# Performance work log

Hardware: AMD Instinct MI355X
Metric: run time of the kernel (lower is better)

## Reference

```python
import jax, jax.numpy as jnp
import numpy as np

EPS = 1e-8  # torch F.cosine_similarity eps


def _gather(features, idx):
    # batched_index_select_tensor: per-batch gather along seq dim
    return jnp.take_along_axis(features, idx[:, :, None], axis=1)


def setup_inputs() -> dict:
    key = jax.random.key(0)
    ks = jax.random.split(key, 7)
    B, S, H, Q, D, C = 8, 512, 768, 64, 256, 2
    return {
        "features": jax.random.normal(ks[0], (B, S, H), dtype=jnp.float32),
        "text_a_indices": jax.random.randint(ks[1], (B, Q), 0, S),
        "text_b_indices": jax.random.randint(ks[2], (B, D), 0, S),
        "W1": jax.random.normal(ks[3], (2 * H, H), dtype=jnp.float32) * 0.02,
        "b1": jax.random.normal(ks[4], (H,), dtype=jnp.float32) * 0.02,
        "W2": jax.random.normal(ks[5], (H, C), dtype=jnp.float32) * 0.02,
        "b2": jax.random.normal(ks[6], (C,), dtype=jnp.float32) * 0.02,
    }


def reference(features, text_a_indices, text_b_indices, W1, b1, W2, b2):
    dt = features.dtype
    a_mask = (text_a_indices > 0).astype(dt)          # [B,Q]
    b_mask = (text_b_indices > 0).astype(dt)          # [B,D]
    a_len = jnp.sum(a_mask, axis=-1)                  # [B]
    b_len = jnp.sum(b_mask, axis=-1)                  # [B]

    q_vec = _gather(features, text_a_indices)         # [B,Q,H]
    d_vec = _gather(features, text_b_indices)         # [B,D,H]

    # cosine similarity with torch eps semantics: x.y / (max(|x|,eps)*max(|y|,eps))
    qn = q_vec / jnp.maximum(jnp.linalg.norm(q_vec, axis=-1, keepdims=True), EPS)
    dn = d_vec / jnp.maximum(jnp.linalg.norm(d_vec, axis=-1, keepdims=True), EPS)
    sim = jnp.einsum("bqh,bdh->bqd", qn, dn)          # [B,Q,D]

    # masked weighted average over doc tokens, per query token (fused; no 4D repeat)
    sim_m = sim * b_mask[:, None, :]
    per_q_doc = jnp.einsum("bqd,bdh->bqh", sim_m, d_vec) / b_len[:, None, None]

    # masked average over query tokens
    am = a_mask[:, :, None]
    query_based_doc = jnp.sum(per_q_doc * am, axis=1) / a_len[:, None]   # [B,H]
    query_avg = jnp.sum(q_vec * am, axis=1) / a_len[:, None]             # [B,H]

    feat = jnp.concatenate([query_avg, query_based_doc], axis=-1)        # [B,2H]
    hidden = jax.nn.relu(feat @ W1 + b1)
    logits = hidden @ W2 + b2
    return logits
```

## Files before the change

### kernel.cpp

```cpp
#include <hip/hip_runtime.h>
#include <hip/hip_bf16.h>

#define B_ 8
#define S_ 512
#define H_ 768
#define Q_ 64
#define D_ 256

__global__ __launch_bounds__(256) void k_norms_lens(
        const float* __restrict__ feats,
        const int* __restrict__ aidx,
        const int* __restrict__ bidx,
        float* __restrict__ invn ,
        float* __restrict__ lens ) {
    int t = threadIdx.x;
    int wave = t >> 6, lane = t & 63;
    if (blockIdx.x < 640) {
        int r = blockIdx.x * 4 + wave;
        int b = r / (Q_ + D_);
        int i = r % (Q_ + D_);
        int idx; float* outp;
        if (i < Q_) {
            idx = aidx[b * Q_ + i];
            outp = invn + b * Q_ + i;
        } else {
            int j = i - Q_;
            idx = bidx[b * D_ + j];
            outp = invn + B_ * Q_ + b * D_ + j;
        }
        const float4* row4 = (const float4*)(feats + ((size_t)b * S_ + idx) * H_);
        float ss = 0.f;
#pragma unroll
        for (int k = 0; k < 3; ++k) {
            float4 v = row4[lane + k * 64];
            ss += v.x * v.x + v.y * v.y + v.z * v.z + v.w * v.w;
        }
        for (int off = 32; off; off >>= 1) ss += __shfl_xor(ss, off, 64);
        if (lane == 0) *outp = 1.f / fmaxf(sqrtf(ss), 1e-8f);
    } else {
        int b = blockIdx.x - 640;
        __shared__ int cnt[4];
        unsigned long long mb = __ballot(bidx[b * D_ + wave * 64 + lane] > 0);
        if (lane == 0) cnt[wave] = __popcll(mb);
        if (wave == 0) {
            unsigned long long ma = __ballot(aidx[b * Q_ + lane] > 0);
            if (lane == 0) lens[b] = (float)__popcll(ma);
        }
        __syncthreads();
        if (t == 0) lens[B_ + b] = (float)(cnt[0] + cnt[1] + cnt[2] + cnt[3]);
    }
}

__global__ __launch_bounds__(256) void k_qbar(
        const float* __restrict__ feats,
        const int* __restrict__ aidx,
        const float* __restrict__ invn,
        const float* __restrict__ lens,
        float* __restrict__ qbar ,
        float* __restrict__ feat ) {
    int b = blockIdx.x / 12;
    int hc = blockIdx.x % 12;
    int t = threadIdx.x;
    int lane = t & 63, qg = t >> 6;
    __shared__ int   s_idx[Q_];
    __shared__ float s_inv[Q_];
    __shared__ float red0[4][64];
    __shared__ float red1[4][64];
    if (t < Q_) {
        s_idx[t] = aidx[b * Q_ + t];
        s_inv[t] = invn[b * Q_ + t];
    }
    __syncthreads();
    int h = hc * 64 + lane;
    float pb = 0.f, pa = 0.f;
#pragma unroll
    for (int q = qg * 16; q < qg * 16 + 16; ++q) {
        int idx = s_idx[q];
        if (idx > 0) {
            float f = feats[((size_t)b * S_ + idx) * H_ + h];
            pb += f * s_inv[q];
            pa += f;
        }
    }
    red0[qg][lane] = pb;
    red1[qg][lane] = pa;
    __syncthreads();
    if (t < 64) {
        int h2 = hc * 64 + t;
        float qb = red0[0][t] + red0[1][t] + red0[2][t] + red0[3][t];
        float qa = red1[0][t] + red1[1][t] + red1[2][t] + red1[3][t];
        qbar[b * H_ + h2] = qb;
        feat[b * 2 * H_ + h2] = qa / lens[b];
    }
}

__global__ __launch_bounds__(256) void k_docw(
        const float* __restrict__ feats,
        const int* __restrict__ bidx,
        const float* __restrict__ invn,
        const float* __restrict__ lens,
        const float* __restrict__ qbar,
        float* __restrict__ w ) {
    int t = threadIdx.x;
    int lane = t & 63;
    int gw = blockIdx.x * 4 + (t >> 6);
    int b = gw >> 8;
    int d = gw & 255;
    int idx = bidx[b * D_ + d];
    const float4* row4 = (const float4*)(feats + ((size_t)b * S_ + idx) * H_);
    const float4* q4 = (const float4*)(qbar + b * H_);
    float dot = 0.f;
#pragma unroll
    for (int k = 0; k < 3; ++k) {
        float4 v = row4[lane + k * 64];
        float4 qv = q4[lane + k * 64];
        dot += v.x * qv.x + v.y * qv.y + v.z * qv.z + v.w * qv.w;
    }
    for (int off = 32; off; off >>= 1) dot += __shfl_xor(dot, off, 64);
    if (lane == 0) {
        float scale = 1.f / (lens[b] * lens[B_ + b]);
        w[b * D_ + d] = (idx > 0) ? dot * invn[B_ * Q_ + b * D_ + d] * scale : 0.f;
    }
}

__global__ __launch_bounds__(256) void k_docsum(
        const float* __restrict__ feats,
        const int* __restrict__ bidx,
        const float* __restrict__ w,
        float* __restrict__ feat) {
    int b = blockIdx.x / 12;
    int hc = blockIdx.x % 12;
    int t = threadIdx.x;
    int lane = t & 63, dg = t >> 6;
    __shared__ float s_w[D_];
    __shared__ int   s_i[D_];
    __shared__ float red[4][64];
    s_w[t] = w[b * D_ + t];
    s_i[t] = bidx[b * D_ + t];
    __syncthreads();
    int h = hc * 64 + lane;
    float acc = 0.f;
#pragma unroll 8
    for (int d = dg * 64; d < dg * 64 + 64; ++d) {
        acc += s_w[d] * feats[((size_t)b * S_ + s_i[d]) * H_ + h];
    }
    red[dg][lane] = acc;
    __syncthreads();
    if (t < 64) {
        feat[b * 2 * H_ + H_ + hc * 64 + t] =
            red[0][t] + red[1][t] + red[2][t] + red[3][t];
    }
}

__global__ __launch_bounds__(256) void k_mlp1(
        const float* __restrict__ feat,
        const float* __restrict__ W1,
        const float* __restrict__ b1,
        float* __restrict__ hidden) {
    int b = blockIdx.x / 12;
    int hc = blockIdx.x % 12;
    int t = threadIdx.x;
    int lane = t & 63, kg = t >> 6;
    __shared__ float s_f[2 * H_];
    __shared__ float red[4][64];
    for (int i = t; i < 2 * H_; i += 256) s_f[i] = feat[b * 2 * H_ + i];
    __syncthreads();
    int h = hc * 64 + lane;
    const float* wp = W1 + (size_t)(kg * 384) * H_ + h;
    const float* fp = s_f + kg * 384;
    float acc = 0.f;
#pragma unroll 8
    for (int k = 0; k < 384; ++k) acc += fp[k] * wp[(size_t)k * H_];
    red[kg][lane] = acc;
    __syncthreads();
    if (t < 64) {
        int h2 = hc * 64 + t;
        float v = red[0][t] + red[1][t] + red[2][t] + red[3][t] + b1[h2];
        hidden[b * H_ + h2] = fmaxf(v, 0.f);
    }
}

__global__ __launch_bounds__(256) void k_mlp2(
        const float* __restrict__ hidden,
        const float* __restrict__ W2,
        const float* __restrict__ b2,
        float* __restrict__ out) {
    int b = blockIdx.x;
    int t = threadIdx.x;
    int lane = t & 63, wave = t >> 6;
    float a0 = 0.f, a1 = 0.f;
#pragma unroll
    for (int k = 0; k < 3; ++k) {
        int h = t + k * 256;
        float v = hidden[b * H_ + h];
        a0 += v * W2[h * 2 + 0];
        a1 += v * W2[h * 2 + 1];
    }
    for (int off = 32; off; off >>= 1) {
        a0 += __shfl_xor(a0, off, 64);
        a1 += __shfl_xor(a1, off, 64);
    }
    __shared__ float r0[4], r1[4];
    if (lane == 0) { r0[wave] = a0; r1[wave] = a1; }
    __syncthreads();
    if (t == 0) {
        out[b * 2 + 0] = r0[0] + r0[1] + r0[2] + r0[3] + b2[0];
        out[b * 2 + 1] = r1[0] + r1[1] + r1[2] + r1[3] + b2[1];
    }
}

extern "C" void kernel_launch(void* const* d_in, const int* in_sizes, int n_in,
                              void* d_out, int out_size, void* d_ws, size_t ws_size,
                              hipStream_t stream) {
    const float* feats = (const float*)d_in[0];
    const int*   aidx  = (const int*)d_in[1];
    const int*   bidx  = (const int*)d_in[2];
    const float* W1    = (const float*)d_in[3];
    const float* b1    = (const float*)d_in[4];
    const float* W2    = (const float*)d_in[5];
    const float* b2    = (const float*)d_in[6];
    float* out = (float*)d_out;

    float* ws = (float*)d_ws;
    float* invn   = ws;
    float* lens   = invn + B_ * (Q_ + D_);
    float* qbar   = lens + 2 * B_;
    float* feat   = qbar + B_ * H_;
    float* w      = feat + B_ * 2 * H_;
    float* hidden = w + B_ * D_;

    k_norms_lens<<<648, 256, 0, stream>>>(feats, aidx, bidx, invn, lens);
    k_qbar<<<96, 256, 0, stream>>>(feats, aidx, invn, lens, qbar, feat);
    k_docw<<<512, 256, 0, stream>>>(feats, bidx, invn, lens, qbar, w);
    k_docsum<<<96, 256, 0, stream>>>(feats, bidx, w, feat);
    k_mlp1<<<96, 256, 0, stream>>>(feat, W1, b1, hidden);
    k_mlp2<<<B_, 256, 0, stream>>>(hidden, W2, b2, out);
}
```

Measured before the change: 114.1 us.

## Fuse six-kernel pipeline into one cooperative kernel with grid-wide syncs

Replaces the chain of six small kernel launches with a single cooperative kernel of 640 blocks that runs each stage in turn, separated by grid.sync(), with shared memory reused through a union. The second MLP layer is folded into the first by reducing within a wavefront and adding atomically into a zeroed output. This targets per-launch overhead and inter-kernel gaps in a tiny, latency-bound workload. In exchange it adds grid barrier cost, atomics that make the summation order nondeterministic, and relies on 640 co-resident blocks, falling back to the old launches if the cooperative launch fails.

New measurement: 396.1 us. 3.47x slower.

```diff
diff --git a/kernel.cpp b/kernel.cpp
--- a/kernel.cpp
+++ b/kernel.cpp
@@ -1,5 +1,8 @@
 #include <hip/hip_runtime.h>
+#include <hip/hip_cooperative_groups.h>
 #include <hip/hip_bf16.h>
+
+namespace cg = cooperative_groups;
 
 #define B_ 8
 #define S_ 512
@@ -7,16 +10,34 @@
 #define Q_ 64
 #define D_ 256
 
-__global__ __launch_bounds__(256) void k_norms_lens(
+__global__ __launch_bounds__(256) void k_fused(
         const float* __restrict__ feats,
         const int* __restrict__ aidx,
         const int* __restrict__ bidx,
+        const float* __restrict__ W1,
+        const float* __restrict__ b1,
+        const float* __restrict__ W2,
+        const float* __restrict__ b2,
         float* __restrict__ invn ,
-        float* __restrict__ lens ) {
-    int t = threadIdx.x;
-    int wave = t >> 6, lane = t & 63;
-    if (blockIdx.x < 640) {
-        int r = blockIdx.x * 4 + wave;
+        float* __restrict__ lens ,
+        float* __restrict__ qbar ,
+        float* __restrict__ feat ,
+        float* __restrict__ w    ,
+        float* __restrict__ out  ) {
+    cg::grid_group grid = cg::this_grid();
+    const int bk = blockIdx.x;
+    const int t  = threadIdx.x;
+    const int wv = t >> 6, lane = t & 63;
+
+    __shared__ union {
+        struct { int cnt[4]; } p1;
+        struct { int idx[Q_]; float inv[Q_]; float red0[4][64]; float red1[4][64]; } p2;
+        struct { float w[D_]; int i[D_]; float red[4][64]; } p4;
+        struct { float f[2 * H_]; float red[4][64]; } p5;
+    } sm;
+
+    {
+        int r = bk * 4 + wv;
         int b = r / (Q_ + D_);
         int i = r % (Q_ + D_);
         int idx; float* outp;
@@ -37,6 +58,151 @@
         }
         for (int off = 32; off; off >>= 1) ss += __shfl_xor(ss, off, 64);
         if (lane == 0) *outp = 1.f / fmaxf(sqrtf(ss), 1e-8f);
+    }
+    if (bk < B_) {
+        int b = bk;
+        unsigned long long mb = __ballot(bidx[b * D_ + wv * 64 + lane] > 0);
+        if (lane == 0) sm.p1.cnt[wv] = __popcll(mb);
+        if (wv == 0) {
+            unsigned long long ma = __ballot(aidx[b * Q_ + lane] > 0);
+            if (lane == 0) lens[b] = (float)__popcll(ma);
+        }
+        __syncthreads();
+        if (t == 0)
+            lens[B_ + b] = (float)(sm.p1.cnt[0] + sm.p1.cnt[1] + sm.p1.cnt[2] + sm.p1.cnt[3]);
+    }
+    if (bk == B_ && t < 2 * B_) out[t] = 0.f;
+
+    grid.sync();
+
+    if (bk < 96) {
+        int b = bk / 12, hc = bk % 12;
+        if (t < Q_) {
+            sm.p2.idx[t] = aidx[b * Q_ + t];
+            sm.p2.inv[t] = invn[b * Q_ + t];
+        }
+        __syncthreads();
+        int h = hc * 64 + lane;
+        float pb = 0.f, pa = 0.f;
+#pragma unroll
+        for (int q = wv * 16; q < wv * 16 + 16; ++q) {
+            int idx = sm.p2.idx[q];
+            if (idx > 0) {
+                float f = feats[((size_t)b * S_ + idx) * H_ + h];
+                pb += f * sm.p2.inv[q];
+                pa += f;
+            }
+        }
+        sm.p2.red0[wv][lane] = pb;
+        sm.p2.red1[wv][lane] = pa;
+        __syncthreads();
+        if (t < 64) {
+            int h2 = hc * 64 + t;
+            float qb = sm.p2.red0[0][t] + sm.p2.red0[1][t] + sm.p2.red0[2][t] + sm.p2.red0[3][t];
+            float qa = sm.p2.red1[0][t] + sm.p2.red1[1][t] + sm.p2.red1[2][t] + sm.p2.red1[3][t];
+            qbar[b * H_ + h2] = qb;
+            feat[b * 2 * H_ + h2] = qa / lens[b];
+        }
+    }
+
+    grid.sync();
+
+    if (bk < 512) {
+        int gw = bk * 4 + wv;
+        int b = gw >> 8;
+        int d = gw & 255;
+        int idx = bidx[b * D_ + d];
+        const float4* row4 = (const float4*)(feats + ((size_t)b * S_ + idx) * H_);
+        const float4* q4 = (const float4*)(qbar + b * H_);
+        float dot = 0.f;
+#pragma unroll
+        for (int k = 0; k < 3; ++k) {
+            float4 v = row4[lane + k * 64];
+            float4 qv = q4[lane + k * 64];
+            dot += v.x * qv.x + v.y * qv.y + v.z * qv.z + v.w * qv.w;
+        }
+        for (int off = 32; off; off >>= 1) dot += __shfl_xor(dot, off, 64);
+        if (lane == 0) {
+            float scale = 1.f / (lens[b] * lens[B_ + b]);
+            w[b * D_ + d] = (idx > 0) ? dot * invn[B_ * Q_ + b * D_ + d] * scale : 0.f;
+        }
+    }
+
+    grid.sync();
+
+    if (bk < 96) {
+        int b = bk / 12, hc = bk % 12;
+        sm.p4.w[t] = w[b * D_ + t];
+        sm.p4.i[t] = bidx[b * D_ + t];
+        __syncthreads();
+        int h = hc * 64 + lane;
+        float acc = 0.f;
+#pragma unroll 8
+        for (int d = wv * 64; d < wv * 64 + 64; ++d) {
+            acc += sm.p4.w[d] * feats[((size_t)b * S_ + sm.p4.i[d]) * H_ + h];
+        }
+        sm.p4.red[wv][lane] = acc;
+        __syncthreads();
+        if (t < 64) {
+            feat[b * 2 * H_ + H_ + hc * 64 + t] =
+                sm.p4.red[0][t] + sm.p4.red[1][t] + sm.p4.red[2][t] + sm.p4.red[3][t];
+        }
+    }
+
+    grid.sync();
+
+    if (bk < 96) {
+        int b = bk / 12, hc = bk % 12;
+        for (int i = t; i < 2 * H_; i += 256) sm.p5.f[i] = feat[b * 2 * H_ + i];
+        __syncthreads();
+        int h = hc * 64 + lane;
+        const float* wp = W1 + (size_t)(wv * 384) * H_ + h;
+        const float* fp = sm.p5.f + wv * 384;
+        float acc = 0.f;
+#pragma unroll 8
+        for (int k = 0; k < 384; ++k) acc += fp[k] * wp[(size_t)k * H_];
+        sm.p5.red[wv][lane] = acc;
+        __syncthreads();
+        if (t < 64) {
+            int h2 = hc * 64 + t;
+            float v = sm.p5.red[0][t] + sm.p5.red[1][t] + sm.p5.red[2][t] + sm.p5.red[3][t] + b1[h2];
+            v = fmaxf(v, 0.f);
+            float p0 = v * W2[h2 * 2 + 0];
+            float p1 = v * W2[h2 * 2 + 1];
+            for (int off = 32; off; off >>= 1) {
+                p0 += __shfl_xor(p0, off, 64);
+                p1 += __shfl_xor(p1, off, 64);
+            }
+            if (t == 0) {
+                atomicAdd(&out[b * 2 + 0], p0 + (hc == 0 ? b2[0] : 0.f));
+                atomicAdd(&out[b * 2 + 1], p1 + (hc == 0 ? b2[1] : 0.f));
+            }
+        }
+    }
+}
+
+__global__ __launch_bounds__(256) void k_norms_lens(
+        const float* __restrict__ feats, const int* __restrict__ aidx,
+        const int* __restrict__ bidx, float* __restrict__ invn,
+        float* __restrict__ lens) {
+    int t = threadIdx.x;
+    int wave = t >> 6, lane = t & 63;
+    if (blockIdx.x < 640) {
+        int r = blockIdx.x * 4 + wave;
+        int b = r / (Q_ + D_);
+        int i = r % (Q_ + D_);
+        int idx; float* outp;
+        if (i < Q_) { idx = aidx[b * Q_ + i]; outp = invn + b * Q_ + i; }
+        else { int j = i - Q_; idx = bidx[b * D_ + j]; outp = invn + B_ * Q_ + b * D_ + j; }
+        const float4* row4 = (const float4*)(feats + ((size_t)b * S_ + idx) * H_);
+        float ss = 0.f;
+#pragma unroll
+        for (int k = 0; k < 3; ++k) {
+            float4 v = row4[lane + k * 64];
+            ss += v.x * v.x + v.y * v.y + v.z * v.z + v.w * v.w;
+        }
+        for (int off = 32; off; off >>= 1) ss += __shfl_xor(ss, off, 64);
+        if (lane == 0) *outp = 1.f / fmaxf(sqrtf(ss), 1e-8f);
     } else {
         int b = blockIdx.x - 640;
         __shared__ int cnt[4];
@@ -52,24 +218,15 @@
 }
 
 __global__ __launch_bounds__(256) void k_qbar(
-        const float* __restrict__ feats,
-        const int* __restrict__ aidx,
-        const float* __restrict__ invn,
-        const float* __restrict__ lens,
-        float* __restrict__ qbar ,
-        float* __restrict__ feat ) {
-    int b = blockIdx.x / 12;
-    int hc = blockIdx.x % 12;
-    int t = threadIdx.x;
-    int lane = t & 63, qg = t >> 6;
-    __shared__ int   s_idx[Q_];
+        const float* __restrict__ feats, const int* __restrict__ aidx,
+        const float* __restrict__ invn, const float* __restrict__ lens,
+        float* __restrict__ qbar, float* __restrict__ feat) {
+    int b = blockIdx.x / 12, hc = blockIdx.x % 12;
+    int t = threadIdx.x, lane = t & 63, qg = t >> 6;
+    __shared__ int s_idx[Q_];
     __shared__ float s_inv[Q_];
-    __shared__ float red0[4][64];
-    __shared__ float red1[4][64];
-    if (t < Q_) {
-        s_idx[t] = aidx[b * Q_ + t];
-        s_inv[t] = invn[b * Q_ + t];
-    }
+    __shared__ float red0[4][64], red1[4][64];
+    if (t < Q_) { s_idx[t] = aidx[b * Q_ + t]; s_inv[t] = invn[b * Q_ + t]; }
     __syncthreads();
     int h = hc * 64 + lane;
     float pb = 0.f, pa = 0.f;
@@ -78,34 +235,25 @@
         int idx = s_idx[q];
         if (idx > 0) {
             float f = feats[((size_t)b * S_ + idx) * H_ + h];
-            pb += f * s_inv[q];
-            pa += f;
-        }
-    }
-    red0[qg][lane] = pb;
-    red1[qg][lane] = pa;
+            pb += f * s_inv[q]; pa += f;
+        }
+    }
+    red0[qg][lane] = pb; red1[qg][lane] = pa;
     __syncthreads();
     if (t < 64) {
         int h2 = hc * 64 + t;
-        float qb = red0[0][t] + red0[1][t] + red0[2][t] + red0[3][t];
-        float qa = red1[0][t] + red1[1][t] + red1[2][t] + red1[3][t];
-        qbar[b * H_ + h2] = qb;
-        feat[b * 2 * H_ + h2] = qa / lens[b];
+        qbar[b * H_ + h2] = red0[0][t] + red0[1][t] + red0[2][t] + red0[3][t];
+        feat[b * 2 * H_ + h2] = (red1[0][t] + red1[1][t] + red1[2][t] + red1[3][t]) / lens[b];
     }
 }
 
 __global__ __launch_bounds__(256) void k_docw(
-        const float* __restrict__ feats,
-        const int* __restrict__ bidx,
-        const float* __restrict__ invn,
-        const float* __restrict__ lens,
-        const float* __restrict__ qbar,
-        float* __restrict__ w ) {
-    int t = threadIdx.x;
-    int lane = t & 63;
+        const float* __restrict__ feats, const int* __restrict__ bidx,
+        const float* __restrict__ invn, const float* __restrict__ lens,
+        const float* __restrict__ qbar, float* __restrict__ w) {
+    int t = threadIdx.x, lane = t & 63;
     int gw = blockIdx.x * 4 + (t >> 6);
-    int b = gw >> 8;
-    int d = gw & 255;
+    int b = gw >> 8, d = gw & 255;
     int idx = bidx[b * D_ + d];
     const float4* row4 = (const float4*)(feats + ((size_t)b * S_ + idx) * H_);
     const float4* q4 = (const float4*)(qbar + b * H_);
@@ -124,16 +272,12 @@
 }
 
 __global__ __launch_bounds__(256) void k_docsum(
-        const float* __restrict__ feats,
-        const int* __restrict__ bidx,
-        const float* __restrict__ w,
-        float* __restrict__ feat) {
-    int b = blockIdx.x / 12;
-    int hc = blockIdx.x % 12;
-    int t = threadIdx.x;
-    int lane = t & 63, dg = t >> 6;
+        const float* __restrict__ feats, const int* __restrict__ bidx,
+        const float* __restrict__ w, float* __restrict__ feat) {
+    int b = blockIdx.x / 12, hc = blockIdx.x % 12;
+    int t = threadIdx.x, lane = t & 63, dg = t >> 6;
     __shared__ float s_w[D_];
-    __shared__ int   s_i[D_];
+    __shared__ int s_i[D_];
     __shared__ float red[4][64];
     s_w[t] = w[b * D_ + t];
     s_i[t] = bidx[b * D_ + t];
@@ -141,26 +285,19 @@
     int h = hc * 64 + lane;
     float acc = 0.f;
 #pragma unroll 8
-    for (int d = dg * 64; d < dg * 64 + 64; ++d) {
+    for (int d = dg * 64; d < dg * 64 + 64; ++d)
         acc += s_w[d] * feats[((size_t)b * S_ + s_i[d]) * H_ + h];
-    }
     red[dg][lane] = acc;
     __syncthreads();
-    if (t < 64) {
-        feat[b * 2 * H_ + H_ + hc * 64 + t] =
-            red[0][t] + red[1][t] + red[2][t] + red[3][t];
-    }
+    if (t < 64)
+        feat[b * 2 * H_ + H_ + hc * 64 + t] = red[0][t] + red[1][t] + red[2][t] + red[3][t];
 }
 
 __global__ __launch_bounds__(256) void k_mlp1(
-        const float* __restrict__ feat,
-        const float* __restrict__ W1,
-        const float* __restrict__ b1,
-        float* __restrict__ hidden) {
-    int b = blockIdx.x / 12;
-    int hc = blockIdx.x % 12;
-    int t = threadIdx.x;
-    int lane = t & 63, kg = t >> 6;
+        const float* __restrict__ feat, const float* __restrict__ W1,
+        const float* __restrict__ b1, float* __restrict__ hidden) {
+    int b = blockIdx.x / 12, hc = blockIdx.x % 12;
+    int t = threadIdx.x, lane = t & 63, kg = t >> 6;
     __shared__ float s_f[2 * H_];
     __shared__ float red[4][64];
     for (int i = t; i < 2 * H_; i += 256) s_f[i] = feat[b * 2 * H_ + i];
@@ -175,19 +312,15 @@
     __syncthreads();
     if (t < 64) {
         int h2 = hc * 64 + t;
-        float v = red[0][t] + red[1][t] + red[2][t] + red[3][t] + b1[h2];
-        hidden[b * H_ + h2] = fmaxf(v, 0.f);
+        hidden[b * H_ + h2] = fmaxf(red[0][t] + red[1][t] + red[2][t] + red[3][t] + b1[h2], 0.f);
     }
 }
 
 __global__ __launch_bounds__(256) void k_mlp2(
-        const float* __restrict__ hidden,
-        const float* __restrict__ W2,
-        const float* __restrict__ b2,
-        float* __restrict__ out) {
+        const float* __restrict__ hidden, const float* __restrict__ W2,
+        const float* __restrict__ b2, float* __restrict__ out) {
     int b = blockIdx.x;
-    int t = threadIdx.x;
-    int lane = t & 63, wave = t >> 6;
+    int t = threadIdx.x, lane = t & 63, wave = t >> 6;
     float a0 = 0.f, a1 = 0.f;
 #pragma unroll
     for (int k = 0; k < 3; ++k) {
@@ -229,10 +362,21 @@
     float* w      = feat + B_ * 2 * H_;
     float* hidden = w + B_ * D_;
 
-    k_norms_lens<<<648, 256, 0, stream>>>(feats, aidx, bidx, invn, lens);
-    k_qbar<<<96, 256, 0, stream>>>(feats, aidx, invn, lens, qbar, feat);
-    k_docw<<<512, 256, 0, stream>>>(feats, bidx, invn, lens, qbar, w);
-    k_docsum<<<96, 256, 0, stream>>>(feats, bidx, w, feat);
-    k_mlp1<<<96, 256, 0, stream>>>(feat, W1, b1, hidden);
-    k_mlp2<<<B_, 256, 0, stream>>>(hidden, W2, b2, out);
-}
+    void* args[] = {
+        (void*)&feats, (void*)&aidx, (void*)&bidx,
+        (void*)&W1, (void*)&b1, (void*)&W2, (void*)&b2,
+        (void*)&invn, (void*)&lens, (void*)&qbar, (void*)&feat, (void*)&w,
+        (void*)&out
+    };
+    hipError_t e = hipLaunchCooperativeKernel((const void*)k_fused,
+                                              dim3(640), dim3(256),
+                                              args, 0, stream);
+    if (e != hipSuccess) {
+        k_norms_lens<<<648, 256, 0, stream>>>(feats, aidx, bidx, invn, lens);
+        k_qbar<<<96, 256, 0, stream>>>(feats, aidx, invn, lens, qbar, feat);
+        k_docw<<<512, 256, 0, stream>>>(feats, bidx, invn, lens, qbar, w);
+        k_docsum<<<96, 256, 0, stream>>>(feats, bidx, w, feat);
+        k_mlp1<<<96, 256, 0, stream>>>(feat, W1, b1, hidden);
+        k_mlp2<<<B_, 256, 0, stream>>>(hidden, W2, b2, out);
+    }
+}
```
